# Kernel tuning notes

Measured on AMD Instinct MI355X. Metric: run time of the kernel, lower is better.

## Reference

```python
import jax, jax.numpy as jnp
import numpy as np

N_HEADS = 16

def setup_inputs() -> dict:
    key = jax.random.key(0)
    ks = jax.random.split(key, 6)
    B, H, F, P, D = 2048, 1024, 4096, 512, 1024
    x = jax.random.normal(ks[0], (B, H), dtype=jnp.float32)
    # module inits features/prototypes ~ U(-0.27, 1)
    features = jax.random.uniform(ks[1], (F, D), minval=-0.27, maxval=1.0, dtype=jnp.float32)
    prototypes = jax.random.uniform(ks[2], (P, D), minval=-0.27, maxval=1.0, dtype=jnp.float32)
    # theta/alpha/beta are zero-init in the module; use small random values so output is non-trivial
    theta = jax.random.normal(ks[3], (N_HEADS, 1), dtype=jnp.float32)
    alpha = jax.random.normal(ks[4], (N_HEADS, 1), dtype=jnp.float32)
    beta = jax.random.normal(ks[5], (N_HEADS, 1), dtype=jnp.float32)
    return {"x": x, "features": features, "prototypes": prototypes,
            "theta": theta, "alpha": alpha, "beta": beta}

def reference(x, features, prototypes, theta, alpha, beta):
    n_heads = N_HEADS
    B, total_dim = x.shape
    d = total_dim // n_heads
    xh = x.reshape(B, n_heads, d)                       # b h d
    fh = features.reshape(-1, n_heads, d).transpose(1, 0, 2)    # h f d
    ph = prototypes.reshape(-1, n_heads, d).transpose(1, 0, 2)  # h p d
    x_features = jnp.einsum('bhd,hfd->bhf', xh, fh)     # [B,h,F]
    p_features = jnp.einsum('hpd,hfd->hpf', ph, fh)     # [h,P,F]
    x_present = jax.nn.relu(x_features)
    p_present = jax.nn.relu(p_features)
    x_weighted = x_features * x_present
    p_weighted = p_features * p_present
    # head-batched GEMMs sharing operands
    common = jnp.einsum('bhf,hpf->bhp', x_weighted, p_weighted)
    x_p_interaction = jnp.einsum('bhf,hpf->bhp', x_weighted, p_present)
    p_x_interaction = jnp.einsum('bhf,hpf->bhp', x_present, p_weighted)
    x_weighted_sum = x_weighted.sum(axis=2, keepdims=True)      # [B,h,1]
    p_weighted_sum = p_weighted.sum(axis=2)[None, :, :]         # [1,h,P]
    x_distinctive = x_weighted_sum - x_p_interaction
    p_distinctive = p_weighted_sum - p_x_interaction
    th = theta.reshape(1, n_heads, 1)
    al = alpha.reshape(1, n_heads, 1)
    be = beta.reshape(1, n_heads, 1)
    out = th * common - al * x_distinctive - be * p_distinctive  # [B,h,P]
    return out.reshape(B, -1)
```

## Files before the change

kernel.cpp:

```cpp
#include <hip/hip_runtime.h>
#include <cstdint>

#define NH 16
#define DH 64
#define FF 4096
#define PP 512
#define BB 2048

typedef __bf16 bf16x8 __attribute__((ext_vector_type(8)));
typedef float f32x4 __attribute__((ext_vector_type(4)));
typedef float fl4 __attribute__((ext_vector_type(4)));
typedef unsigned short us4 __attribute__((ext_vector_type(4)));
typedef unsigned int u32x2 __attribute__((ext_vector_type(2)));

__device__ __forceinline__ unsigned short f2bf(float f) {
  unsigned u = __float_as_uint(f);
  u += 0x7FFFu + ((u >> 16) & 1u);
  return (unsigned short)(u >> 16);
}

__device__ __forceinline__ unsigned int pkbf(float lo, float hi) {
  unsigned a = __float_as_uint(lo) + 0x8000u;
  unsigned b = __float_as_uint(hi) + 0x8000u;
  return __builtin_amdgcn_perm(b, a, 0x07060302u);
}

__device__ __forceinline__ void gload_lds16(const void* g, void* l) {
  __builtin_amdgcn_global_load_lds(
      (const __attribute__((address_space(1))) void*)g,
      (__attribute__((address_space(3))) void*)(unsigned int)(unsigned long long)l,
      16, 0, 0);
}

__global__ void cvt_fp(const float* __restrict__ f, const float* __restrict__ p,
                       unsigned short* __restrict__ fb,
                       unsigned short* __restrict__ pb) {
  const int nf = FF * 1024 / 4, np = PP * 1024 / 4;
  int i = blockIdx.x * blockDim.x + threadIdx.x;
  const fl4* src;
  us4* dst;
  if (i < nf) {
    src = (const fl4*)f + i;
    dst = (us4*)fb + i;
  } else if (i < nf + np) {
    src = (const fl4*)p + (i - nf);
    dst = (us4*)pb + (i - nf);
  } else {
    return;
  }
  fl4 v = *src;
  us4 o;
  o.x = f2bf(v.x); o.y = f2bf(v.y); o.z = f2bf(v.z); o.w = f2bf(v.w);
  *dst = o;
}

__global__ __launch_bounds__(256, 2) void gemm_proto(
    const unsigned short* __restrict__ Abf, const unsigned short* __restrict__ Fbf,
    unsigned short* __restrict__ O1, unsigned short* __restrict__ O2,
    float* __restrict__ pws,
    const float* __restrict__ theta, const float* __restrict__ alpha,
    const float* __restrict__ beta) {
  const int h = blockIdx.z;
  const int n0 = blockIdx.x * 128;
  const int lm0 = blockIdx.y * 128;
  const int t = threadIdx.x;

  __shared__ __align__(16) char As[128 * 128];
  __shared__ __align__(16) char Bs[128 * 128];

  {
    const char* ab = (const char*)(Abf + (size_t)lm0 * 1024 + h * 64);
    const char* bb = (const char*)(Fbf + (size_t)n0 * 1024 + h * 64);
#pragma unroll
    for (int r = 0; r < 4; ++r) {
      int o = r * 4096 + t * 16;
      int row = o >> 7, col = o & 127;
      gload_lds16(ab + (size_t)row * 2048 + col, As + o);
      gload_lds16(bb + (size_t)row * 2048 + col, Bs + o);
    }
  }
  __syncthreads();

  const int wave = t >> 6, lane = t & 63;
  const int wm = wave & 1, wn = wave >> 1;
  const int quad = lane >> 4, lr = lane & 15;

  f32x4 acc[4][4];
#pragma unroll
  for (int i = 0; i < 4; ++i)
#pragma unroll
    for (int j = 0; j < 4; ++j) acc[i][j] = (f32x4){0.f, 0.f, 0.f, 0.f};

#pragma unroll
  for (int s = 0; s < 2; ++s) {
    bf16x8 av[4], bv[4];
#pragma unroll
    for (int fm = 0; fm < 4; ++fm) {
      int row = wm * 64 + fm * 16 + lr;
      av[fm] = *(const bf16x8*)(As + row * 128 + s * 64 + quad * 16);
    }
#pragma unroll
    for (int fn = 0; fn < 4; ++fn) {
      int row = wn * 64 + fn * 16 + lr;
      bv[fn] = *(const bf16x8*)(Bs + row * 128 + s * 64 + quad * 16);
    }
#pragma unroll
    for (int fm = 0; fm < 4; ++fm)
#pragma unroll
      for (int fn = 0; fn < 4; ++fn)
        acc[fm][fn] = __builtin_amdgcn_mfma_f32_16x16x32_bf16(av[fm], bv[fn],
                                                              acc[fm][fn], 0, 0, 0);
  }

  const float th = theta[h], al = alpha[h], be = beta[h];

#pragma unroll
  for (int fm = 0; fm < 4; ++fm) {
    int prow = lm0 + wm * 64 + fm * 16 + quad * 4;
    float rs0 = 0.f, rs1 = 0.f, rs2 = 0.f, rs3 = 0.f;
#pragma unroll
    for (int fn = 0; fn < 4; ++fn) {
      int f = n0 + wn * 64 + fn * 16 + lr;
#pragma unroll
      for (int i = 0; i < 4; ++i) {
        float pf = acc[fm][fn][i];
        float pp = fmaxf(pf, 0.f);
        float pw = pf * pp;
        size_t idx = ((size_t)(h * PP + prow + i)) * FF + f;
        O1[idx] = f2bf(th * pw + al * pp - al);
        O2[idx] = f2bf(be * pw);
        if (i == 0) rs0 += pw;
        else if (i == 1) rs1 += pw;
        else if (i == 2) rs2 += pw;
        else rs3 += pw;
      }
    }
    float rs[4] = {rs0, rs1, rs2, rs3};
#pragma unroll
    for (int i = 0; i < 4; ++i) {
      float s = rs[i];
      s += __shfl_xor(s, 1);
      s += __shfl_xor(s, 2);
      s += __shfl_xor(s, 4);
      s += __shfl_xor(s, 8);
      if (lr == 0) atomicAdd(&pws[h * PP + prow + i], be * s);
    }
  }
}

__global__ __launch_bounds__(256, 2) void fused_main(
    const float* __restrict__ x, const unsigned short* __restrict__ f_bf,
    const unsigned short* __restrict__ Q1, const unsigned short* __restrict__ Q2,
    const float* __restrict__ pws, float* __restrict__ out) {
  const int h = blockIdx.z;
  const int n0 = blockIdx.x * 256;
  const int m0 = blockIdx.y * 128;
  const int t = threadIdx.x;
  const int wave = t >> 6, lane = t & 63;
  const int wm = wave & 1, wn = wave >> 1;
  const int quad = lane >> 4, lr = lane & 15;
  const int key8 = lr & 7;
  const int key2 = (lr >> 1) & 3;

  __shared__ __align__(16) char sF[4096];
  __shared__ __align__(16) char sQ1[16384];
  __shared__ __align__(16) char sQ2[16384];
  __shared__ __align__(16) char sXw[8192];
  __shared__ __align__(16) char sXp[8192];

  bf16x8 xh[2][2];
#pragma unroll
  for (int bn = 0; bn < 2; ++bn)
#pragma unroll
    for (int s = 0; s < 2; ++s) {
      int b = m0 + wave * 32 + bn * 16 + lr;
      const float* xr = x + (size_t)b * 1024 + h * 64 + s * 32 + quad * 8;
      fl4 v0 = *(const fl4*)xr;
      fl4 v1 = *(const fl4*)(xr + 4);
      union { unsigned u[4]; bf16x8 v; } cv;
      cv.u[0] = pkbf(v0.x, v0.y);
      cv.u[1] = pkbf(v0.z, v0.w);
      cv.u[2] = pkbf(v1.x, v1.y);
      cv.u[3] = pkbf(v1.z, v1.w);
      xh[bn][s] = cv.v;
    }

  int af_off[2][2];
#pragma unroll
  for (int fm = 0; fm < 2; ++fm)
#pragma unroll
    for (int s = 0; s < 2; ++s)
      af_off[fm][s] = (fm * 16 + lr) * 128 + (((s * 4 + quad) ^ key8) * 16);

  int cw_off[2][2];
#pragma unroll
  for (int fm = 0; fm < 2; ++fm)
#pragma unroll
    for (int bn = 0; bn < 2; ++bn)
      cw_off[fm][bn] = (wave * 32 + bn * 16 + lr) * 64 +
                       (((fm * 2 + (quad >> 1)) ^ key2) * 16) + (quad & 1) * 8;

  int aw_off[4];
#pragma unroll
  for (int fm = 0; fm < 4; ++fm)
    aw_off[fm] = (wm * 64 + fm * 16 + lr) * 64 + ((quad ^ key2) * 16);

  int bq_off[8];
#pragma unroll
  for (int fn = 0; fn < 8; ++fn)
    bq_off[fn] = (wn * 128 + fn * 16 + lr) * 64 + ((quad ^ key2) * 16);

  const char* srcF;
  {
    int row = t >> 3, c = t & 7, cs = c ^ (row & 7);
    srcF = (const char*)f_bf + h * 128 + (size_t)row * 2048 + cs * 16;
  }
  const char* srcQ1[4];
  const char* srcQ2[4];
  {
    const char* q1b = (const char*)(Q1 + ((size_t)h * PP + n0) * FF);
    const char* q2b = (const char*)(Q2 + ((size_t)h * PP + n0) * FF);
#pragma unroll
    for (int r = 0; r < 4; ++r) {
      int ci = r * 256 + t, row = ci >> 2, c = ci & 3, cs = c ^ ((row >> 1) & 3);
      srcQ1[r] = q1b + (size_t)row * 8192 + cs * 16;
      srcQ2[r] = q2b + (size_t)row * 8192 + cs * 16;
    }
  }

  f32x4 acc[4][8];
#pragma unroll
  for (int i = 0; i < 4; ++i)
#pragma unroll
    for (int j = 0; j < 8; ++j) acc[i][j] = (f32x4){0.f, 0.f, 0.f, 0.f};

  for (int it = 0; it < FF / 32; ++it) {
    __syncthreads();
    gload_lds16(srcF, sF + t * 16);
    srcF += 32 * 2048;
#pragma unroll
    for (int r = 0; r < 4; ++r) {
      gload_lds16(srcQ1[r], sQ1 + r * 4096 + t * 16);
      gload_lds16(srcQ2[r], sQ2 + r * 4096 + t * 16);
      srcQ1[r] += 64;
      srcQ2[r] += 64;
    }
    __syncthreads();

    f32x4 xf[2][2];
#pragma unroll
    for (int fm = 0; fm < 2; ++fm)
#pragma unroll
      for (int bn = 0; bn < 2; ++bn) xf[fm][bn] = (f32x4){0.f, 0.f, 0.f, 0.f};
#pragma unroll
    for (int s = 0; s < 2; ++s)
#pragma unroll
      for (int fm = 0; fm < 2; ++fm) {
        bf16x8 af = *(const bf16x8*)(sF + af_off[fm][s]);
#pragma unroll
        for (int bn = 0; bn < 2; ++bn)
          xf[fm][bn] = __builtin_amdgcn_mfma_f32_16x16x32_bf16(af, xh[bn][s],
                                                               xf[fm][bn], 0, 0, 0);
      }

#pragma unroll
    for (int fm = 0; fm < 2; ++fm)
#pragma unroll
      for (int bn = 0; bn < 2; ++bn) {
        float v0 = xf[fm][bn][0], v1 = xf[fm][bn][1];
        float v2 = xf[fm][bn][2], v3 = xf[fm][bn][3];
        float p0 = fmaxf(v0, 0.f), p1 = fmaxf(v1, 0.f);
        float p2 = fmaxf(v2, 0.f), p3 = fmaxf(v3, 0.f);
        u32x2 w, p;
        w.x = pkbf(v0 * p0, v1 * p1);
        w.y = pkbf(v2 * p2, v3 * p3);
        p.x = pkbf(p0, p1);
        p.y = pkbf(p2, p3);
        *(u32x2*)(sXw + cw_off[fm][bn]) = w;
        *(u32x2*)(sXp + cw_off[fm][bn]) = p;
      }
    __syncthreads();

    bf16x8 aw[4], ap[4];
#pragma unroll
    for (int fm = 0; fm < 4; ++fm) {
      aw[fm] = *(const bf16x8*)(sXw + aw_off[fm]);
      ap[fm] = *(const bf16x8*)(sXp + aw_off[fm]);
    }
#pragma unroll
    for (int fn = 0; fn < 8; ++fn) {
      bf16x8 b1 = *(const bf16x8*)(sQ1 + bq_off[fn]);
      bf16x8 b2 = *(const bf16x8*)(sQ2 + bq_off[fn]);
#pragma unroll
      for (int fm = 0; fm < 4; ++fm) {
        acc[fm][fn] = __builtin_amdgcn_mfma_f32_16x16x32_bf16(aw[fm], b1,
                                                              acc[fm][fn], 0, 0, 0);
        acc[fm][fn] = __builtin_amdgcn_mfma_f32_16x16x32_bf16(ap[fm], b2,
                                                              acc[fm][fn], 0, 0, 0);
      }
    }
  }

#pragma unroll
  for (int fn = 0; fn < 8; ++fn) {
    int p = n0 + wn * 128 + fn * 16 + lr;
    float sub = pws[h * PP + p];
#pragma unroll
    for (int fm = 0; fm < 4; ++fm) {
      int brow = m0 + wm * 64 + fm * 16 + quad * 4;
#pragma unroll
      for (int i = 0; i < 4; ++i) {
        out[(size_t)(brow + i) * (NH * PP) + h * PP + p] = acc[fm][fn][i] - sub;
      }
    }
  }
}

extern "C" void kernel_launch(void* const* d_in, const int* in_sizes, int n_in,
                              void* d_out, int out_size, void* d_ws, size_t ws_size,
                              hipStream_t stream) {
  const float* x = (const float*)d_in[0];
  const float* features = (const float*)d_in[1];
  const float* prototypes = (const float*)d_in[2];
  const float* theta = (const float*)d_in[3];
  const float* alpha = (const float*)d_in[4];
  const float* beta = (const float*)d_in[5];
  float* out = (float*)d_out;

  char* ws = (char*)d_ws;
  size_t off = 0;
  auto carve = [&](size_t bytes) -> char* {
    char* p = ws + off;
    off += (bytes + 255) & ~(size_t)255;
    return p;
  };
  unsigned short* f_bf = (unsigned short*)carve((size_t)FF * 1024 * 2);
  unsigned short* p_bf = (unsigned short*)carve((size_t)PP * 1024 * 2);
  unsigned short* Q1 = (unsigned short*)carve((size_t)NH * PP * FF * 2);
  unsigned short* Q2 = (unsigned short*)carve((size_t)NH * PP * FF * 2);
  float* pws = (float*)carve((size_t)NH * PP * 4);

  const int ncvt = (FF + PP) * 1024 / 4;
  cvt_fp<<<(ncvt + 255) / 256, 256, 0, stream>>>(features, prototypes, f_bf, p_bf);
  hipMemsetAsync(pws, 0, (size_t)NH * PP * 4, stream);

  gemm_proto<<<dim3(FF / 128, PP / 128, NH), 256, 0, stream>>>(
      p_bf, f_bf, Q1, Q2, pws, theta, alpha, beta);

  fused_main<<<dim3(PP / 256, BB / 128, NH), 256, 0, stream>>>(
      x, f_bf, Q1, Q2, pws, out);
}
```

Baseline: 408.1 us.

## Load Q operands directly to registers and double-buffer feature tile in LDS

The main fused kernel stops staging the Q1/Q2 prototype tiles through shared memory. Each wave now reads its own 64 prototype rows straight into registers, and the warp tiling is reorganised so every wave covers all 128 batch rows. The feature tile is double-buffered in LDS with a prefetch one iteration ahead, and one full barrier per iteration is removed, with setprio raised around the MFMA block. The intent is to cut LDS traffic and barrier stalls, at the cost of global-load latency that is exposed directly to registers and higher register pressure. The workspace is padded by one tile so the final prefetch stays in bounds.

```diff
diff --git a/kernel.cpp b/kernel.cpp
--- a/kernel.cpp
+++ b/kernel.cpp
@@ -157,14 +157,11 @@
   const int m0 = blockIdx.y * 128;
   const int t = threadIdx.x;
   const int wave = t >> 6, lane = t & 63;
-  const int wm = wave & 1, wn = wave >> 1;
   const int quad = lane >> 4, lr = lane & 15;
   const int key8 = lr & 7;
   const int key2 = (lr >> 1) & 3;
 
-  __shared__ __align__(16) char sF[4096];
-  __shared__ __align__(16) char sQ1[16384];
-  __shared__ __align__(16) char sQ2[16384];
+  __shared__ __align__(16) char sF[2 * 4096];
   __shared__ __align__(16) char sXw[8192];
   __shared__ __align__(16) char sXp[8192];
 
@@ -200,52 +197,47 @@
       cw_off[fm][bn] = (wave * 32 + bn * 16 + lr) * 64 +
                        (((fm * 2 + (quad >> 1)) ^ key2) * 16) + (quad & 1) * 8;
 
-  int aw_off[4];
-#pragma unroll
-  for (int fm = 0; fm < 4; ++fm)
-    aw_off[fm] = (wm * 64 + fm * 16 + lr) * 64 + ((quad ^ key2) * 16);
-
-  int bq_off[8];
-#pragma unroll
-  for (int fn = 0; fn < 8; ++fn)
-    bq_off[fn] = (wn * 128 + fn * 16 + lr) * 64 + ((quad ^ key2) * 16);
+  int aw_off[8];
+#pragma unroll
+  for (int fm = 0; fm < 8; ++fm)
+    aw_off[fm] = (fm * 16 + lr) * 64 + ((quad ^ key2) * 16);
 
   const char* srcF;
   {
     int row = t >> 3, c = t & 7, cs = c ^ (row & 7);
     srcF = (const char*)f_bf + h * 128 + (size_t)row * 2048 + cs * 16;
   }
-  const char* srcQ1[4];
-  const char* srcQ2[4];
-  {
-    const char* q1b = (const char*)(Q1 + ((size_t)h * PP + n0) * FF);
-    const char* q2b = (const char*)(Q2 + ((size_t)h * PP + n0) * FF);
-#pragma unroll
-    for (int r = 0; r < 4; ++r) {
-      int ci = r * 256 + t, row = ci >> 2, c = ci & 3, cs = c ^ ((row >> 1) & 3);
-      srcQ1[r] = q1b + (size_t)row * 8192 + cs * 16;
-      srcQ2[r] = q2b + (size_t)row * 8192 + cs * 16;
-    }
-  }
-
-  f32x4 acc[4][8];
-#pragma unroll
-  for (int i = 0; i < 4; ++i)
-#pragma unroll
-    for (int j = 0; j < 8; ++j) acc[i][j] = (f32x4){0.f, 0.f, 0.f, 0.f};
+
+  const unsigned short* qrow1 =
+      Q1 + (size_t)(h * PP + n0 + wave * 64 + lr) * FF + quad * 8;
+  const unsigned short* qrow2 =
+      Q2 + (size_t)(h * PP + n0 + wave * 64 + lr) * FF + quad * 8;
+
+  f32x4 acc[8][4];
+#pragma unroll
+  for (int i = 0; i < 8; ++i)
+#pragma unroll
+    for (int j = 0; j < 4; ++j) acc[i][j] = (f32x4){0.f, 0.f, 0.f, 0.f};
+
+  gload_lds16(srcF, sF + t * 16);
+  srcF += 32 * 2048;
+  asm volatile("s_waitcnt vmcnt(0)\n\ts_barrier" ::: "memory");
+  __builtin_amdgcn_sched_barrier(0);
 
   for (int it = 0; it < FF / 32; ++it) {
-    __syncthreads();
-    gload_lds16(srcF, sF + t * 16);
+    const int cur = (it & 1) << 12;
+
+    bf16x8 q1v[4], q2v[4];
+#pragma unroll
+    for (int fn = 0; fn < 4; ++fn) {
+      q1v[fn] = *(const bf16x8*)(qrow1 + fn * (16 * FF));
+      q2v[fn] = *(const bf16x8*)(qrow2 + fn * (16 * FF));
+    }
+    qrow1 += 32;
+    qrow2 += 32;
+
+    gload_lds16(srcF, sF + (cur ^ 4096) + t * 16);
     srcF += 32 * 2048;
-#pragma unroll
-    for (int r = 0; r < 4; ++r) {
-      gload_lds16(srcQ1[r], sQ1 + r * 4096 + t * 16);
-      gload_lds16(srcQ2[r], sQ2 + r * 4096 + t * 16);
-      srcQ1[r] += 64;
-      srcQ2[r] += 64;
-    }
-    __syncthreads();
 
     f32x4 xf[2][2];
 #pragma unroll
@@ -256,7 +248,7 @@
     for (int s = 0; s < 2; ++s)
 #pragma unroll
       for (int fm = 0; fm < 2; ++fm) {
-        bf16x8 af = *(const bf16x8*)(sF + af_off[fm][s]);
+        bf16x8 af = *(const bf16x8*)(sF + cur + af_off[fm][s]);
 #pragma unroll
         for (int bn = 0; bn < 2; ++bn)
           xf[fm][bn] = __builtin_amdgcn_mfma_f32_16x16x32_bf16(af, xh[bn][s],
@@ -279,35 +271,41 @@
         *(u32x2*)(sXw + cw_off[fm][bn]) = w;
         *(u32x2*)(sXp + cw_off[fm][bn]) = p;
       }
-    __syncthreads();
-
-    bf16x8 aw[4], ap[4];
-#pragma unroll
-    for (int fm = 0; fm < 4; ++fm) {
-      aw[fm] = *(const bf16x8*)(sXw + aw_off[fm]);
-      ap[fm] = *(const bf16x8*)(sXp + aw_off[fm]);
-    }
-#pragma unroll
-    for (int fn = 0; fn < 8; ++fn) {
-      bf16x8 b1 = *(const bf16x8*)(sQ1 + bq_off[fn]);
-      bf16x8 b2 = *(const bf16x8*)(sQ2 + bq_off[fn]);
+    asm volatile("s_waitcnt lgkmcnt(0)\n\ts_barrier" ::: "memory");
+    __builtin_amdgcn_sched_barrier(0);
+
+    __builtin_amdgcn_s_setprio(1);
+#pragma unroll
+    for (int hf = 0; hf < 2; ++hf) {
+      bf16x8 aw[4], ap[4];
 #pragma unroll
       for (int fm = 0; fm < 4; ++fm) {
-        acc[fm][fn] = __builtin_amdgcn_mfma_f32_16x16x32_bf16(aw[fm], b1,
-                                                              acc[fm][fn], 0, 0, 0);
-        acc[fm][fn] = __builtin_amdgcn_mfma_f32_16x16x32_bf16(ap[fm], b2,
-                                                              acc[fm][fn], 0, 0, 0);
-      }
-    }
-  }
-
-#pragma unroll
-  for (int fn = 0; fn < 8; ++fn) {
-    int p = n0 + wn * 128 + fn * 16 + lr;
+        aw[fm] = *(const bf16x8*)(sXw + aw_off[hf * 4 + fm]);
+        ap[fm] = *(const bf16x8*)(sXp + aw_off[hf * 4 + fm]);
+      }
+#pragma unroll
+      for (int fn = 0; fn < 4; ++fn)
+#pragma unroll
+        for (int fm = 0; fm < 4; ++fm) {
+          acc[hf * 4 + fm][fn] = __builtin_amdgcn_mfma_f32_16x16x32_bf16(
+              aw[fm], q1v[fn], acc[hf * 4 + fm][fn], 0, 0, 0);
+          acc[hf * 4 + fm][fn] = __builtin_amdgcn_mfma_f32_16x16x32_bf16(
+              ap[fm], q2v[fn], acc[hf * 4 + fm][fn], 0, 0, 0);
+        }
+    }
+    __builtin_amdgcn_s_setprio(0);
+
+    asm volatile("s_waitcnt vmcnt(0)\n\ts_barrier" ::: "memory");
+    __builtin_amdgcn_sched_barrier(0);
+  }
+
+#pragma unroll
+  for (int fn = 0; fn < 4; ++fn) {
+    int p = n0 + wave * 64 + fn * 16 + lr;
     float sub = pws[h * PP + p];
 #pragma unroll
-    for (int fm = 0; fm < 4; ++fm) {
-      int brow = m0 + wm * 64 + fm * 16 + quad * 4;
+    for (int fm = 0; fm < 8; ++fm) {
+      int brow = m0 + fm * 16 + quad * 4;
 #pragma unroll
       for (int i = 0; i < 4; ++i) {
         out[(size_t)(brow + i) * (NH * PP) + h * PP + p] = acc[fm][fn][i] - sub;
@@ -334,7 +332,7 @@
     off += (bytes + 255) & ~(size_t)255;
     return p;
   };
-  unsigned short* f_bf = (unsigned short*)carve((size_t)FF * 1024 * 2);
+  unsigned short* f_bf = (unsigned short*)carve((size_t)(FF + 32) * 1024 * 2);
   unsigned short* p_bf = (unsigned short*)carve((size_t)PP * 1024 * 2);
   unsigned short* Q1 = (unsigned short*)carve((size_t)NH * PP * FF * 2);
   unsigned short* Q2 = (unsigned short*)carve((size_t)NH * PP * FF * 2);
```

New measurement: 386.0 us. -5.4%, faster.
